# Kernel optimization log

Hardware: AMD Instinct MI355X
Metric: run time of the kernel (lower is better)

Reference implementation:

```python
import jax, jax.numpy as jnp
import numpy as np

B, S, D, NL = 512, 200, 128, 2
N_ITEMS = 50001
DH = 2 * D
DFF = 4 * D


def layer_norm(x, g, b, eps=1e-5):
    mu = x.mean(-1, keepdims=True)
    v = ((x - mu) ** 2).mean(-1, keepdims=True)
    return (x - mu) / jnp.sqrt(v + eps) * g + b


def lru_scan(h, lamb0, mask):
    # h: (B, L, DH) complex64, lamb0: (DH,) complex64, mask: (B, L) bool
    Bb, L, Dh = h.shape
    log2_L = int(np.ceil(np.log2(L)))
    lamb = lamb0.reshape(1, Dh)
    for i in range(1, log2_L + 1):
        l = 2 ** i
        h = h.reshape(Bb * L // l, l, Dh)
        m = mask.reshape(Bb * L // l, l)
        h1, h2 = h[:, : l // 2], h[:, l // 2:]
        if i > 1:
            lamb = jnp.concatenate([lamb, lamb * lamb[-1]], axis=0)  # powers lambda^1..lambda^(l/2)
        carry_gate = m[:, l // 2 - 1 : l // 2, None].astype(h.dtype)
        h2 = h2 + lamb * h1[:, -1:] * carry_gate
        h = jnp.concatenate([h1, h2], axis=1)
    return h.reshape(Bb, L, Dh)


def _forward(token_emb, emb_ln_g, emb_ln_b, params_log,
             in_wr, in_wi, in_br, in_bi, out_wr, out_wi, out_br, out_bi,
             lru_ln_g, lru_ln_b, w1, b1, w2, b2, ffn_ln_g, ffn_ln_b,
             item_seq, item_seq_len):
    mask = item_seq > 0                      # (B, S)
    x = token_emb[item_seq]                  # (B, S, D)
    x = layer_norm(x, emb_ln_g, emb_ln_b)
    seq_len = item_seq.shape[1]
    L = 2 ** int(np.ceil(np.log2(seq_len)))
    pad = L - seq_len
    x = jnp.pad(x, ((0, 0), (pad, 0), (0, 0)))        # left-pad seq to power of 2
    m = jnp.pad(mask, ((0, 0), (pad, 0)))
    n_layers = params_log.shape[0]
    for li in range(n_layers):
        pl = jnp.exp(params_log[li])                  # (3, DH): nu, theta, gamma
        nu, theta, gamma = pl[0], pl[1], pl[2]
        lamb0 = jnp.exp(jax.lax.complex(-nu, theta))  # (DH,)
        in_w = jax.lax.complex(in_wr[li], in_wi[li])
        in_b = jax.lax.complex(in_br[li], in_bi[li])
        h = (jnp.einsum('bld,hd->blh', x.astype(jnp.complex64), in_w) + in_b) * gamma
        h = lru_scan(h, lamb0, m)
        out_w = jax.lax.complex(out_wr[li], out_wi[li])
        out_b = jax.lax.complex(out_br[li], out_bi[li])
        y = (jnp.einsum('blh,dh->bld', h, out_w) + out_b).real + x
        x = layer_norm(y, lru_ln_g[li], lru_ln_b[li])
        # positionwise FFN with residual + post-LN
        hff = jax.nn.gelu(jnp.einsum('bld,fd->blf', x, w1[li]) + b1[li], approximate=False)
        x = layer_norm(jnp.einsum('blf,df->bld', hff, w2[li]) + b2[li] + x,
                       ffn_ln_g[li], ffn_ln_b[li])
    x = x[:, -seq_len:]                               # (B, S, D)
    idx = item_seq_len - 1
    return x[jnp.arange(x.shape[0]), idx]             # (B, D)


def setup_inputs() -> dict:
    key = jax.random.key(0)
    ks = jax.random.split(key, 24)
    std = 0.02
    item_seq = jax.random.randint(ks[0], (B, S), 0, N_ITEMS)
    item_seq_len = jax.random.randint(ks[1], (B,), 1, S + 1)
    # LRU diagonal init (matches torch init)
    r_min, r_max = 0.8, 0.99
    u1 = jax.random.uniform(ks[2], (NL, DH))
    u2 = jax.random.uniform(ks[3], (NL, DH))
    nu_log = jnp.log(-0.5 * jnp.log(u1 * (r_max ** 2 - r_min ** 2) + r_min ** 2))
    theta_log = jnp.log(u2 * 2.0 * np.pi)
    gamma_log = 0.5 * jnp.log(1.0 - jnp.exp(-2.0 * jnp.exp(nu_log)))
    params_log = jnp.stack([nu_log, theta_log, gamma_log], axis=1)  # (NL, 3, DH)
    rn = lambda k, sh: jax.random.normal(k, sh, dtype=jnp.float32) * std
    return {
        'token_emb': rn(ks[4], (N_ITEMS, D)),
        'emb_ln_g': jnp.ones((D,), jnp.float32), 'emb_ln_b': jnp.zeros((D,), jnp.float32),
        'params_log': params_log,
        'in_wr': rn(ks[5], (NL, DH, D)), 'in_wi': rn(ks[6], (NL, DH, D)),
        'in_br': rn(ks[7], (NL, DH)), 'in_bi': rn(ks[8], (NL, DH)),
        'out_wr': rn(ks[9], (NL, D, DH)), 'out_wi': rn(ks[10], (NL, D, DH)),
        'out_br': rn(ks[11], (NL, D)), 'out_bi': rn(ks[12], (NL, D)),
        'lru_ln_g': jnp.ones((NL, D), jnp.float32), 'lru_ln_b': jnp.zeros((NL, D), jnp.float32),
        'w1': rn(ks[13], (NL, DFF, D)), 'b1': rn(ks[14], (NL, DFF)),
        'w2': rn(ks[15], (NL, D, DFF)), 'b2': rn(ks[16], (NL, D)),
        'ffn_ln_g': jnp.ones((NL, D), jnp.float32), 'ffn_ln_b': jnp.zeros((NL, D), jnp.float32),
        'item_seq': item_seq, 'item_seq_len': item_seq_len,
    }


def reference(token_emb, emb_ln_g, emb_ln_b, params_log,
              in_wr, in_wi, in_br, in_bi, out_wr, out_wi, out_br, out_bi,
              lru_ln_g, lru_ln_b, w1, b1, w2, b2, ffn_ln_g, ffn_ln_b,
              item_seq, item_seq_len):
    return _forward(token_emb, emb_ln_g, emb_ln_b, params_log,
                    in_wr, in_wi, in_br, in_bi, out_wr, out_wi, out_br, out_bi,
                    lru_ln_g, lru_ln_b, w1, b1, w2, b2, ffn_ln_g, ffn_ln_b,
                    item_seq, item_seq_len)
```

## Files before the change

### kernel.cpp

```cpp
#include <hip/hip_runtime.h>
#include <hip/hip_bf16.h>
#include <math.h>

#define B_TOT 512
#define SEQ   200
#define D     128
#define DH    256
#define DFF   512
#define LPAD  256
#define PADL  56
#define NLAY  2
#define SSTRIP 140

typedef __attribute__((ext_vector_type(8))) short bf16x8;
typedef __attribute__((ext_vector_type(4))) float floatx4;
typedef __attribute__((ext_vector_type(2))) float floatx2;

static __device__ inline float bf2f(ushort u) {
    union { unsigned int i; float f; } v; v.i = ((unsigned int)u) << 16; return v.f;
}
static __device__ inline ushort f2bf(float x) {
    union { float f; unsigned int i; } v; v.f = x;
    unsigned int r = (v.i + 0x7FFFu + ((v.i >> 16) & 1u)) >> 16;
    return (ushort)r;
}
static __device__ inline unsigned int pkbf(float a, float b) {
    union { __hip_bfloat162 h; unsigned int u; } v;
    v.h = __float22bfloat162_rn(make_float2(a, b));
    return v.u;
}
static __device__ inline void gld_lds16(const void* g, void* l) {
    __builtin_amdgcn_global_load_lds(
        (const __attribute__((address_space(1))) unsigned int*)g,
        (__attribute__((address_space(3))) unsigned int*)l, 16, 0, 0);
}

static __device__ inline size_t haddr(int b, int s, int k) {
    int p  = k >> 8;
    int ch = k & 255;
    int g  = ch >> 5;
    int cl = ch & 31;
    return (((((size_t)b * 8 + g) * 2 + p) * SEQ + s) * 32 + cl);
}

__global__ void setup_all_kernel(const float* __restrict__ params_log,
                                 const float* __restrict__ in_br,
                                 const float* __restrict__ in_bi,
                                 const float* __restrict__ in_wr,
                                 const float* __restrict__ in_wi,
                                 const float* __restrict__ out_wr,
                                 const float* __restrict__ out_wi,
                                 const float* __restrict__ w1,
                                 const float* __restrict__ w2,
                                 ushort* __restrict__ Winb,
                                 ushort* __restrict__ W2effb,
                                 ushort* __restrict__ w1b,
                                 ushort* __restrict__ w2b,
                                 float* __restrict__ lam_pow,
                                 float* __restrict__ scale_in,
                                 float* __restrict__ bias_in)
{
    int idx = blockIdx.x * blockDim.x + threadIdx.x;
    int li = idx >> 16;
    int e  = idx & 65535;

    {
        int gp = e >> 12, rem = e & 4095;
        int q = rem >> 3, e8 = rem & 7;
        int r = q >> 4, cs = q & 15;
        int c16 = cs ^ (r & 7);
        int n = (r < 16) ? (gp * 16 + r) : (256 + gp * 16 + (r - 16));
        int d = c16 * 8 + e8;
        float wv = (n < DH) ? in_wr[((size_t)li * DH + n) * D + d]
                            : in_wi[((size_t)li * DH + (n - DH)) * D + d];
        Winb[idx] = f2bf(wv);
    }
    {
        int k0c = e >> 13, rem = e & 8191;
        int q = rem >> 3, e8 = rem & 7;
        int r = q >> 3, cs = q & 7;
        int c16 = cs ^ (r & 7);
        int k = k0c * 64 + c16 * 8 + e8;
        float w2v = (k < DH) ? out_wr[((size_t)li * D + r) * DH + k]
                             : -out_wi[((size_t)li * D + r) * DH + (k - DH)];
        W2effb[idx] = f2bf(w2v);
    }
    {
        int row = e >> 7, col = e & 127;
        int ffc = row >> 7, rl = row & 127;
        int c16 = col >> 3, e8 = col & 7;
        int cs = c16 ^ (rl & 7);
        w1b[li * 65536 + ffc * 16384 + rl * 128 + cs * 8 + e8] = f2bf(w1[idx]);
    }
    {
        int dd2 = e >> 9, kk = e & 511;
        int ffc = kk >> 7, klc = kk & 127;
        int c16 = klc >> 3, e8 = klc & 7;
        int cs = c16 ^ (dd2 & 7);
        w2b[li * 65536 + ffc * 16384 + dd2 * 128 + cs * 8 + e8] = f2bf(w2[idx]);
    }

    if (blockIdx.x < NLAY) {
        int pli = blockIdx.x;
        int c = threadIdx.x;
        const float* pl = params_log + (size_t)pli * 3 * DH;
        float nu = expf(pl[c]);
        float th = expf(pl[DH + c]);
        float ga = expf(pl[2 * DH + c]);
        float mag = expf(-nu);
        float lr = mag * cosf(th);
        float lim = mag * sinf(th);
        float2* lp = (float2*)(lam_pow + (size_t)pli * 65536) + (size_t)c * 128;
        float pr = lr, pi = lim;
        lp[0] = make_float2(pr, pi);
        for (int k = 1; k < 128; ++k) {
            float nr = pr * lr - pi * lim;
            float ni = pr * lim + pi * lr;
            pr = nr; pi = ni;
            lp[k] = make_float2(pr, pi);
        }
        scale_in[pli * 2 * DH + c]      = ga;
        scale_in[pli * 2 * DH + DH + c] = ga;
        bias_in[pli * 2 * DH + c]       = in_br[pli * DH + c] * ga;
        bias_in[pli * 2 * DH + DH + c]  = in_bi[pli * DH + c] * ga;
    }
}

__global__ __launch_bounds__(256) void embed_ln_kernel(
    const float* __restrict__ emb, const int* __restrict__ seq,
    const int* __restrict__ lenp,
    const float* __restrict__ g, const float* __restrict__ bt,
    ushort* __restrict__ x,
    int Bc, int* __restrict__ total, int* __restrict__ rowmap)
{
    if (blockIdx.x == gridDim.x - 1) {
        __shared__ int ps[257];
        int t = threadIdx.x;
        int b0_ = 2 * t, b1_ = 2 * t + 1;
        int lv0 = (b0_ < Bc) ? lenp[b0_] : 0;
        int lv1 = (b1_ < Bc) ? lenp[b1_] : 0;
        ps[t + 1] = lv0 + lv1;
        if (t == 0) ps[0] = 0;
        __syncthreads();
        for (int ofs = 1; ofs < 256; ofs <<= 1) {
            int v = ps[t + 1];
            int vv = (t + 1 > ofs) ? ps[t + 1 - ofs] : 0;
            __syncthreads();
            ps[t + 1] = v + vv;
            __syncthreads();
        }
        if (t == 255) total[0] = ps[256];
        int base = ps[t];
        int rb0 = b0_ * SEQ, rb1 = b1_ * SEQ;
        for (int s = 0; s < lv0; ++s) rowmap[base + s] = rb0 + s;
        base += lv0;
        for (int s = 0; s < lv1; ++s) rowmap[base + s] = rb1 + s;
        return;
    }
    int row  = blockIdx.x * 4 + (threadIdx.x >> 6);
    int lane = threadIdx.x & 63;
    int b = row / SEQ, s = row - b * SEQ;
    if (s >= lenp[b]) return;
    int item = seq[row];
    float2 v = *(const float2*)(emb + (size_t)item * D + lane * 2);
    float ssum = v.x + v.y;
#pragma unroll
    for (int o = 32; o > 0; o >>= 1) ssum += __shfl_xor(ssum, o);
    float mu = ssum * (1.0f / D);
    float d0 = v.x - mu, d1 = v.y - mu;
    float vs = d0 * d0 + d1 * d1;
#pragma unroll
    for (int o = 32; o > 0; o >>= 1) vs += __shfl_xor(vs, o);
    float rstd = rsqrtf(vs * (1.0f / D) + 1e-5f);
    float2 gg = *(const float2*)(g + lane * 2);
    float2 bb = *(const float2*)(bt + lane * 2);
    unsigned int o2 = pkbf(d0 * rstd * gg.x + bb.x, d1 * rstd * gg.y + bb.y);
    *(unsigned int*)(x + (size_t)row * D + lane * 2) = o2;
}

template <bool LAST>
__global__ __launch_bounds__(512) void inproj_scan_kernel(
    const ushort* __restrict__ X, const ushort* __restrict__ Win,
    ushort* __restrict__ H, const float2* __restrict__ lamT,
    const int* __restrict__ seq, const int* __restrict__ lenp,
    const float* __restrict__ scale_in, const float* __restrict__ bias_in)
{
    __shared__ __align__(16) char smem[36864];
    __shared__ __align__(16) float mkfS[32 * 12];
    char*  Wsm = smem;
    char*  xs  = smem + 8192;
    float* stR2 = (float*)smem;
    float* stI2 = stR2 + 32 * SSTRIP;

    int gp = blockIdx.x, b = blockIdx.y;
    int tid = threadIdx.x;
    int l = tid & 63, w = tid >> 6;
    int ct = w & 1;
    int rq = w >> 1;
    int lr = l & 15, lq = l >> 4;
    int wbase = tid & ~63;

    int c  = tid >> 5;
    int tl = tid & 31;
    int t0 = tl * 8;
    int lbase = l & 32;
    int coff = (c >> 2) * 36 + (c & 3) * 8;

    int s_b = lenp[b] - 1;
    int tile_max = s_b >> 4;
    int nrows = (tile_max + 1) * 16;
    int tb = s_b + PADL;
    bool activeT = (t0 <= tb);

    const ushort* xrow = X + (size_t)b * SEQ * 128;
    gld_lds16(Win + (size_t)gp * 4096 + (size_t)tid * 8,
              Wsm + (size_t)wbase * 16);
    int nrA = nrows < 112 ? nrows : 112;
#pragma unroll
    for (int it = 0; it < 4; ++it) {
        int rbase = it * 32 + w * 4;
        int r = rbase + lq;
        int cs = lr ^ (r & 7);
        if (r < nrA)
            gld_lds16(xrow + (size_t)r * 128 + cs * 8, xs + rbase * 256);
    }

    const float2* myl = lamT + (size_t)(gp * 16 + c) * 128;

    if (tid < LPAD) {
        int t = tid;
        float m = 0.f;
        if (t >= PADL) m = (seq[(size_t)b * SEQ + (t - PADL)] > 0) ? 1.f : 0.f;
        mkfS[(t >> 3) * 12 + (t & 7)] = m;
    }
    __syncthreads();

    bf16x8 wf[4];
#pragma unroll
    for (int kk = 0; kk < 4; ++kk) {
        int ca = kk * 4 + lq;
        int wr = ct * 16 + lr;
        wf[kk] = *(const bf16x8*)(Wsm + wr * 256 + ((ca ^ (wr & 7)) * 16));
    }
    int tstart = rq ? (3 * rq + 1) : 0;
    int tcnt   = rq ? 3 : 4;
    floatx4 acc[4];
#pragma unroll
    for (int tt = 0; tt < 4; ++tt) acc[tt] = (floatx4)0.f;

    if (rq < 2) {
#pragma unroll
        for (int tt = 0; tt < 4; ++tt) {
            if (tt < tcnt && (tstart + tt) <= tile_max) {
                int t  = tstart + tt;
                int ar = t * 16 + lr;
#pragma unroll
                for (int kk = 0; kk < 4; ++kk) {
                    int ca = kk * 4 + lq;
                    bf16x8 af = *(const bf16x8*)(xs + ar * 256 + ((ca ^ (ar & 7)) * 16));
                    acc[tt] = __builtin_amdgcn_mfma_f32_16x16x32_bf16(wf[kk], af, acc[tt], 0, 0, 0);
                }
            }
        }
    }
    __syncthreads();

    if (nrows > 112) {
        int nrB = nrows < 200 ? nrows : 200;
#pragma unroll
        for (int it = 0; it < 3; ++it) {
            int rbase = it * 32 + w * 4;
            int rl_ = rbase + lq;
            int gr = 112 + rl_;
            int cs = lr ^ (rl_ & 7);
            if (gr < nrB)
                gld_lds16(xrow + (size_t)gr * 128 + cs * 8, xs + rbase * 256);
        }
    }
    __syncthreads();

    if (rq >= 2) {
#pragma unroll
        for (int tt = 0; tt < 4; ++tt) {
            if (tt < tcnt && (tstart + tt) <= tile_max) {
                int t  = tstart + tt;
                int ar = (t - 7) * 16 + lr;
#pragma unroll
                for (int kk = 0; kk < 4; ++kk) {
                    int ca = kk * 4 + lq;
                    bf16x8 af = *(const bf16x8*)(xs + ar * 256 + ((ca ^ (ar & 7)) * 16));
                    acc[tt] = __builtin_amdgcn_mfma_f32_16x16x32_bf16(wf[kk], af, acc[tt], 0, 0, 0);
                }
            }
        }
    }
    __syncthreads();

    float2 l14[4];
#pragma unroll
    for (int k = 0; k < 4; ++k) l14[k] = myl[k];
    float2 myl9 = myl[8];
    float2 lam_e[3];
#pragma unroll
    for (int i = 0; i < 3; ++i) {
        int half = 32 << i;
        int off = t0 & ((half << 1) - 1);
        int e = off - half;
        lam_e[i] = myl[e < 0 ? 0 : e];
    }
    float2 l7;
    l7.x = l14[3].x * l14[2].x - l14[3].y * l14[2].y;
    l7.y = l14[3].x * l14[2].y + l14[3].y * l14[2].x;

    for (int idx = tid; idx < 7 * SSTRIP; idx += 512) { stR2[idx] = 0.f; stI2[idx] = 0.f; }
    {
        float4 g4 = *(const float4*)(scale_in + ct * 256 + gp * 16 + lq * 4);
        float4 b4 = *(const float4*)(bias_in  + ct * 256 + gp * 16 + lq * 4);
        float* base = ct ? stI2 : stR2;
#pragma unroll
        for (int tt = 0; tt < 4; ++tt) {
            if (tt < tcnt && (tstart + tt) <= tile_max) {
                int t = tstart + tt;
                int s = t * 16 + lr;
                if (s <= s_b) {
                    float* dst = base + (2 * t + 7 + (lr >> 3)) * SSTRIP
                               + lq * 36 + (lr & 7);
                    dst[0]  = acc[tt][0] * g4.x + b4.x;
                    dst[8]  = acc[tt][1] * g4.y + b4.y;
                    dst[16] = acc[tt][2] * g4.z + b4.z;
                    dst[24] = acc[tt][3] * g4.w + b4.w;
                }
            }
        }
    }
    __syncthreads();

    floatx2 Xr[4], Xi[4], Mf[4];
    {
        const float* pr = stR2 + tl * SSTRIP + coff;
        const float* pi = stI2 + tl * SSTRIP + coff;
        floatx4 r0 = *(const floatx4*)pr;
        floatx4 r1 = *(const floatx4*)(pr + 4);
        floatx4 i0 = *(const floatx4*)pi;
        floatx4 i1 = *(const floatx4*)(pi + 4);
        floatx4 m0 = *(const floatx4*)(mkfS + tl * 12);
        floatx4 m1 = *(const floatx4*)(mkfS + tl * 12 + 4);
        Xr[0] = floatx2{r0[0], r0[1]}; Xr[1] = floatx2{r0[2], r0[3]};
        Xr[2] = floatx2{r1[0], r1[1]}; Xr[3] = floatx2{r1[2], r1[3]};
        Xi[0] = floatx2{i0[0], i0[1]}; Xi[1] = floatx2{i0[2], i0[3]};
        Xi[2] = floatx2{i1[0], i1[1]}; Xi[3] = floatx2{i1[2], i1[3]};
        Mf[0] = floatx2{m0[0], m0[1]}; Mf[1] = floatx2{m0[2], m0[3]};
        Mf[2] = floatx2{m1[0], m1[1]}; Mf[3] = floatx2{m1[2], m1[3]};
    }

    float l0x = l14[0].x, l0y = l14[0].y;
    floatx2 L01R = floatx2{l14[0].x, l14[1].x};
    floatx2 L01I = floatx2{l14[0].y, l14[1].y};
    floatx2 L23R = floatx2{l14[2].x, l14[3].x};
    floatx2 L23I = floatx2{l14[2].y, l14[3].y};

    if (activeT) {
#pragma unroll
        for (int p = 0; p < 4; ++p) {
            float sr = Xr[p].x * Mf[p].x, si = Xi[p].x * Mf[p].x;
            Xr[p].y += l0x * sr; Xr[p].y -= l0y * si;
            Xi[p].y += l0x * si; Xi[p].y += l0y * sr;
        }
#pragma unroll
        for (int p = 0; p < 2; ++p) {
            int sp_ = p * 2;
            float sr = Xr[sp_].y * Mf[sp_].y, si = Xi[sp_].y * Mf[sp_].y;
            Xr[sp_ + 1] += sr * L01R; Xr[sp_ + 1] -= si * L01I;
            Xi[sp_ + 1] += si * L01R; Xi[sp_ + 1] += sr * L01I;
        }
        {
            float sr = Xr[1].y * Mf[1].y, si = Xi[1].y * Mf[1].y;
            Xr[2] += sr * L01R; Xr[2] -= si * L01I;
            Xi[2] += si * L01R; Xi[2] += sr * L01I;
            Xr[3] += sr * L23R; Xr[3] -= si * L23I;
            Xi[3] += si * L23R; Xi[3] += sr * L23I;
        }
    }

    float x7r, x7i;
    if (activeT) { x7r = Xr[3].y; x7i = Xi[3].y; }
    else         { x7r = 0.f;     x7i = 0.f; }
    float Ctr = 0.f, Cti = 0.f;
    float m7 = Mf[3].y;
    float pxr = x7r * m7, pxi = x7i * m7;

#define TREE_LEVEL(SRC_TL, TGT, LE)                                          \
    {                                                                        \
        int srcl = lbase | (SRC_TL);                                         \
        float svx = __shfl(pxr, srcl);                                       \
        float svy = __shfl(pxi, srcl);                                       \
        if (activeT && (TGT)) {                                              \
            float2 le = (LE);                                                \
            float cr = le.x * svx - le.y * svy;                              \
            float ci = le.x * svy + le.y * svx;                              \
            Ctr += cr; Cti += ci;                                            \
            x7r += l7.x * cr - l7.y * ci;                                    \
            x7i += l7.x * ci + l7.y * cr;                                    \
            pxr = x7r * m7; pxi = x7i * m7;                                  \
        }                                                                    \
    }

    TREE_LEVEL(tl & ~1,          tl & 1,  l14[0]);
    TREE_LEVEL((tl & ~3)  | 1,   tl & 2,  (tl & 1) ? myl9 : l14[0]);
    TREE_LEVEL((tl & ~7)  | 3,   tl & 4,  lam_e[0]);
    if (tb >= 64)  TREE_LEVEL((tl & ~15) | 7,  tl & 8,  lam_e[1]);
    if (tb >= 128) TREE_LEVEL((tl & ~31) | 15, tl & 16, lam_e[2]);
#undef TREE_LEVEL

    if (activeT && (!LAST || (unsigned)(tb - t0) < 7u)) {
        float2 l5, l6;
        l5.x = l14[3].x * l14[0].x - l14[3].y * l14[0].y;
        l5.y = l14[3].x * l14[0].y + l14[3].y * l14[0].x;
        l6.x = l14[3].x * l14[1].x - l14[3].y * l14[1].y;
        l6.y = l14[3].x * l14[1].y + l14[3].y * l14[1].x;
        Xr[0].x += Ctr;                                 Xi[0].x += Cti;
        Xr[0].y += l14[0].x * Ctr; Xr[0].y -= l14[0].y * Cti;
        Xi[0].y += l14[0].x * Cti; Xi[0].y += l14[0].y * Ctr;
        Xr[1].x += l14[1].x * Ctr; Xr[1].x -= l14[1].y * Cti;
        Xi[1].x += l14[1].x * Cti; Xi[1].x += l14[1].y * Ctr;
        Xr[1].y += l14[2].x * Ctr; Xr[1].y -= l14[2].y * Cti;
        Xi[1].y += l14[2].x * Cti; Xi[1].y += l14[2].y * Ctr;
        Xr[2].x += l14[3].x * Ctr; Xr[2].x -= l14[3].y * Cti;
        Xi[2].x += l14[3].x * Cti; Xi[2].x += l14[3].y * Ctr;
        Xr[2].y += l5.x * Ctr;     Xr[2].y -= l5.y * Cti;
        Xi[2].y += l5.x * Cti;     Xi[2].y += l5.y * Ctr;
        Xr[3].x += l6.x * Ctr;     Xr[3].x -= l6.y * Cti;
        Xi[3].x += l6.x * Cti;     Xi[3].x += l6.y * Ctr;
    }
    Xr[3].y = x7r; Xi[3].y = x7i;

    if (LAST) {
        if (activeT && (unsigned)(tb - t0) < 8u) {
#pragma unroll
            for (int k = 0; k < 8; ++k)
                if (t0 + k == tb) {
                    float vr = (k & 1) ? Xr[k >> 1].y : Xr[k >> 1].x;
                    float vi = (k & 1) ? Xi[k >> 1].y : Xi[k >> 1].x;
                    stR2[tl * SSTRIP + coff + k] = vr;
                    stI2[tl * SSTRIP + coff + k] = vi;
                }
        }
    } else {
        if (activeT && tl >= 7) {
            floatx4 r0 = floatx4{Xr[0].x, Xr[0].y, Xr[1].x, Xr[1].y};
            floatx4 r1 = floatx4{Xr[2].x, Xr[2].y, Xr[3].x, Xr[3].y};
            floatx4 i0 = floatx4{Xi[0].x, Xi[0].y, Xi[1].x, Xi[1].y};
            floatx4 i1 = floatx4{Xi[2].x, Xi[2].y, Xi[3].x, Xi[3].y};
            *(floatx4*)(stR2 + tl * SSTRIP + coff)     = r0;
            *(floatx4*)(stR2 + tl * SSTRIP + coff + 4) = r1;
            *(floatx4*)(stI2 + tl * SSTRIP + coff)     = i0;
            *(floatx4*)(stI2 + tl * SSTRIP + coff + 4) = i1;
        }
    }
    __syncthreads();

    if (LAST) {
        if (tid < 32) {
            int p = tid >> 4, cc = tid & 15;
            int fi = (tb >> 3) * SSTRIP + (cc >> 2) * 36 + (cc & 3) * 8 + (tb & 7);
            float v = (p ? stI2 : stR2)[fi];
            H[(size_t)b * 512 + p * 256 + gp * 16 + cc] = f2bf(v);
        }
    } else {
        int g  = gp >> 1;
        int hc = (gp & 1) * 16;
        ushort* baseg = H + (size_t)(b * 8 + g) * 2 * SEQ * 32 + hc;
#pragma unroll
        for (int it = 0; it < 4; ++it) {
            int idx4 = it * 512 + tid;
            if (idx4 < 2 * SEQ * 4) {
                int q  = idx4 & 3;
                int ps = idx4 >> 2;
                int p  = ps >= SEQ;
                int s  = ps - p * SEQ;
                if (s > s_b) continue;
                const float* sp = (p ? stI2 : stR2)
                                + ((s + PADL) >> 3) * SSTRIP + q * 36 + (s & 7);
                float a0 = sp[0], a1 = sp[8], a2 = sp[16], a3 = sp[24];
                uint2 raw;
                raw.x = pkbf(a0, a1);
                raw.y = pkbf(a2, a3);
                *(uint2*)(baseg + (size_t)ps * 32 + q * 4) = raw;
            }
        }
    }
}

__global__ __launch_bounds__(256) void outproj_kernel(
    const ushort* __restrict__ A, const ushort* __restrict__ Wimg,
    ushort* __restrict__ Cout,
    const int* __restrict__ rowmap, const int* __restrict__ totalp,
    const float* __restrict__ e0,
    const ushort* __restrict__ res,
    const float* __restrict__ lng, const float* __restrict__ lnb)
{
    int m0 = blockIdx.x * 64;
    int total = totalp[0];
    if (m0 >= total) return;
    __shared__ __align__(16) char As[8192];
    __shared__ __align__(16) char Bs[16384];
    __shared__ float2 lnS[2][64];
    int tid = threadIdx.x;
    int l = tid & 63, w = tid >> 6;
    int chh = w >> 1;
    int rh  = w & 1;
    int lr = l & 15, lq = l >> 4;
    int wbase = tid & ~63;

    int cst = tid & 7;
    int rr  = tid >> 3;
    int sb[2], ss[2];
#pragma unroll
    for (int it = 0; it < 2; ++it) {
        int gr = m0 + it * 32 + rr;
        if (gr >= total) gr = total - 1;
        int rm = rowmap[gr];
        sb[it] = rm / SEQ; ss[it] = rm - sb[it] * SEQ;
    }

    floatx4 acc[4][2];
#pragma unroll
    for (int i = 0; i < 4; ++i)
#pragma unroll
        for (int j = 0; j < 2; ++j) acc[i][j] = (floatx4)0.f;

    for (int k0c = 0; k0c < 8; ++k0c) {
        int k0 = k0c * 64;
        {
            const ushort* img = Wimg + (size_t)k0c * 8192;
#pragma unroll
            for (int it = 0; it < 4; ++it)
                gld_lds16(img + (size_t)(it * 256 + tid) * 8,
                          Bs + (size_t)(it * 256 + wbase) * 16);
        }
#pragma unroll
        for (int it = 0; it < 2; ++it) {
            int r = it * 32 + rr;
            uint4 va = *(const uint4*)(A + haddr(sb[it], ss[it], k0 + cst * 8));
            *(uint4*)(As + r * 128 + ((cst ^ (r & 7)) * 16)) = va;
        }
        __syncthreads();
#pragma unroll
        for (int kk = 0; kk < 2; ++kk) {
            bf16x8 wf[4], af[2];
            int ca = kk * 4 + lq;
#pragma unroll
            for (int i = 0; i < 4; ++i) {
                int rb = chh * 64 + i * 16 + lr;
                wf[i] = *(const bf16x8*)(Bs + rb * 128 + ((ca ^ (rb & 7)) * 16));
            }
#pragma unroll
            for (int j = 0; j < 2; ++j) {
                int ra = rh * 32 + j * 16 + lr;
                af[j] = *(const bf16x8*)(As + ra * 128 + ((ca ^ (ra & 7)) * 16));
            }
#pragma unroll
            for (int i = 0; i < 4; ++i)
#pragma unroll
                for (int j = 0; j < 2; ++j)
                    acc[i][j] = __builtin_amdgcn_mfma_f32_16x16x32_bf16(
                        wf[i], af[j], acc[i][j], 0, 0, 0);
        }
        __syncthreads();
    }

    int chb[4], arow[2], rmj[2];
#pragma unroll
    for (int i = 0; i < 4; ++i) chb[i] = chh * 64 + i * 16 + lq * 4;
#pragma unroll
    for (int j = 0; j < 2; ++j) {
        arow[j] = m0 + rh * 32 + j * 16 + lr;
        int rc = arow[j] < total ? arow[j] : total - 1;
        rmj[j] = rowmap[rc];
    }

    {
        float4 bias[4], gv[4], bv[4];
#pragma unroll
        for (int i = 0; i < 4; ++i) {
            bias[i] = *(const float4*)(e0 + chb[i]);
            gv[i]   = *(const float4*)(lng + chb[i]);
            bv[i]   = *(const float4*)(lnb + chb[i]);
        }
#pragma unroll
        for (int j = 0; j < 2; ++j) {
#pragma unroll
            for (int i = 0; i < 4; ++i) {
                ushort4 r4 = *(const ushort4*)(res + (size_t)rmj[j] * 128 + chb[i]);
                acc[i][j][0] += ((const float*)&bias[i])[0] + bf2f(r4.x);
                acc[i][j][1] += ((const float*)&bias[i])[1] + bf2f(r4.y);
                acc[i][j][2] += ((const float*)&bias[i])[2] + bf2f(r4.z);
                acc[i][j][3] += ((const float*)&bias[i])[3] + bf2f(r4.w);
            }
        }
#pragma unroll
        for (int j = 0; j < 2; ++j) {
            float s = 0.f, q = 0.f;
#pragma unroll
            for (int i = 0; i < 4; ++i)
#pragma unroll
                for (int reg = 0; reg < 4; ++reg) {
                    float v = acc[i][j][reg];
                    s += v; q += v * v;
                }
            s += __shfl_xor(s, 16); q += __shfl_xor(q, 16);
            s += __shfl_xor(s, 32); q += __shfl_xor(q, 32);
            if (lq == 0) lnS[chh][rh * 32 + j * 16 + lr] = make_float2(s, q);
        }
        __syncthreads();
#pragma unroll
        for (int j = 0; j < 2; ++j) {
            int rl = rh * 32 + j * 16 + lr;
            float2 s0 = lnS[0][rl], s1 = lnS[1][rl];
            float mu  = (s0.x + s1.x) * (1.0f / 128.0f);
            float var = (s0.y + s1.y) * (1.0f / 128.0f) - mu * mu;
            float rstd = rsqrtf(var + 1e-5f);
            if (arow[j] < total) {
#pragma unroll
                for (int i = 0; i < 4; ++i) {
                    uint2 u;
                    u.x = pkbf((acc[i][j][0] - mu) * rstd * ((const float*)&gv[i])[0] + ((const float*)&bv[i])[0],
                               (acc[i][j][1] - mu) * rstd * ((const float*)&gv[i])[1] + ((const float*)&bv[i])[1]);
                    u.y = pkbf((acc[i][j][2] - mu) * rstd * ((const float*)&gv[i])[2] + ((const float*)&bv[i])[2],
                               (acc[i][j][3] - mu) * rstd * ((const float*)&gv[i])[3] + ((const float*)&bv[i])[3]);
                    *(uint2*)(Cout + (size_t)rmj[j] * 128 + chb[i]) = u;
                }
            }
        }
    }
}

__global__ __launch_bounds__(256) void outproj_last_kernel(
    const ushort* __restrict__ Hc, const ushort* __restrict__ Wimg,
    ushort* __restrict__ xc, int Bc,
    const float* __restrict__ e0,
    const ushort* __restrict__ Xres, const int* __restrict__ lenp,
    const float* __restrict__ lng, const float* __restrict__ lnb)
{
    __shared__ __align__(16) char As[8192];
    __shared__ __align__(16) char Bs[16384];
    __shared__ float2 lnS[2][64];
    int tid = threadIdx.x;
    int l = tid & 63, w = tid >> 6;
    int chh = w >> 1;
    int rh  = w & 1;
    int lr = l & 15, lq = l >> 4;
    int m0 = blockIdx.x * 64;
    int wbase = tid & ~63;

    int cst = tid & 7;
    int rr  = tid >> 3;

    floatx4 acc[4][2];
#pragma unroll
    for (int i = 0; i < 4; ++i)
#pragma unroll
        for (int j = 0; j < 2; ++j) acc[i][j] = (floatx4)0.f;

    for (int k0c = 0; k0c < 8; ++k0c) {
        int k0 = k0c * 64;
        {
            const ushort* img = Wimg + (size_t)k0c * 8192;
#pragma unroll
            for (int it = 0; it < 4; ++it)
                gld_lds16(img + (size_t)(it * 256 + tid) * 8,
                          Bs + (size_t)(it * 256 + wbase) * 16);
        }
#pragma unroll
        for (int it = 0; it < 2; ++it) {
            int r = it * 32 + rr;
            int gr = m0 + r; if (gr >= Bc) gr = Bc - 1;
            uint4 va = *(const uint4*)(Hc + (size_t)gr * 512 + k0 + cst * 8);
            *(uint4*)(As + r * 128 + ((cst ^ (r & 7)) * 16)) = va;
        }
        __syncthreads();
#pragma unroll
        for (int kk = 0; kk < 2; ++kk) {
            bf16x8 wf[4], af[2];
            int ca = kk * 4 + lq;
#pragma unroll
            for (int i = 0; i < 4; ++i) {
                int rb = chh * 64 + i * 16 + lr;
                wf[i] = *(const bf16x8*)(Bs + rb * 128 + ((ca ^ (rb & 7)) * 16));
            }
#pragma unroll
            for (int j = 0; j < 2; ++j) {
                int ra = rh * 32 + j * 16 + lr;
                af[j] = *(const bf16x8*)(As + ra * 128 + ((ca ^ (ra & 7)) * 16));
            }
#pragma unroll
            for (int i = 0; i < 4; ++i)
#pragma unroll
                for (int j = 0; j < 2; ++j)
                    acc[i][j] = __builtin_amdgcn_mfma_f32_16x16x32_bf16(
                        wf[i], af[j], acc[i][j], 0, 0, 0);
        }
        __syncthreads();
    }

    int chb[4], arow[2];
#pragma unroll
    for (int i = 0; i < 4; ++i) chb[i] = chh * 64 + i * 16 + lq * 4;
#pragma unroll
    for (int j = 0; j < 2; ++j) arow[j] = m0 + rh * 32 + j * 16 + lr;

    {
        float4 bias[4], gv[4], bv[4];
#pragma unroll
        for (int i = 0; i < 4; ++i) {
            bias[i] = *(const float4*)(e0 + chb[i]);
            gv[i]   = *(const float4*)(lng + chb[i]);
            bv[i]   = *(const float4*)(lnb + chb[i]);
        }
#pragma unroll
        for (int j = 0; j < 2; ++j) {
            int br = arow[j] < Bc ? arow[j] : Bc - 1;
            int sb_ = lenp[br] - 1;
            const ushort* rbase = Xres + ((size_t)br * SEQ + sb_) * 128;
#pragma unroll
            for (int i = 0; i < 4; ++i) {
                ushort4 r4 = *(const ushort4*)(rbase + chb[i]);
                acc[i][j][0] += ((const float*)&bias[i])[0] + bf2f(r4.x);
                acc[i][j][1] += ((const float*)&bias[i])[1] + bf2f(r4.y);
                acc[i][j][2] += ((const float*)&bias[i])[2] + bf2f(r4.z);
                acc[i][j][3] += ((const float*)&bias[i])[3] + bf2f(r4.w);
            }
        }
#pragma unroll
        for (int j = 0; j < 2; ++j) {
            float s = 0.f, q = 0.f;
#pragma unroll
            for (int i = 0; i < 4; ++i)
#pragma unroll
                for (int reg = 0; reg < 4; ++reg) {
                    float v = acc[i][j][reg];
                    s += v; q += v * v;
                }
            s += __shfl_xor(s, 16); q += __shfl_xor(q, 16);
            s += __shfl_xor(s, 32); q += __shfl_xor(q, 32);
            if (lq == 0) lnS[chh][rh * 32 + j * 16 + lr] = make_float2(s, q);
        }
        __syncthreads();
#pragma unroll
        for (int j = 0; j < 2; ++j) {
            int rl = rh * 32 + j * 16 + lr;
            float2 s0 = lnS[0][rl], s1 = lnS[1][rl];
            float mu  = (s0.x + s1.x) * (1.0f / 128.0f);
            float var = (s0.y + s1.y) * (1.0f / 128.0f) - mu * mu;
            float rstd = rsqrtf(var + 1e-5f);
            if (arow[j] < Bc) {
#pragma unroll
                for (int i = 0; i < 4; ++i) {
                    uint2 u;
                    u.x = pkbf((acc[i][j][0] - mu) * rstd * ((const float*)&gv[i])[0] + ((const float*)&bv[i])[0],
                               (acc[i][j][1] - mu) * rstd * ((const float*)&gv[i])[1] + ((const float*)&bv[i])[1]);
                    u.y = pkbf((acc[i][j][2] - mu) * rstd * ((const float*)&gv[i])[2] + ((const float*)&bv[i])[2],
                               (acc[i][j][3] - mu) * rstd * ((const float*)&gv[i])[3] + ((const float*)&bv[i])[3]);
                    *(uint2*)(xc + (size_t)arow[j] * 128 + chb[i]) = u;
                }
            }
        }
    }
}

__global__ __launch_bounds__(256) void ffn_fused_kernel(
    ushort* __restrict__ X, const ushort* __restrict__ W1,
    const ushort* __restrict__ W2,
    const float* __restrict__ b1, const float* __restrict__ b2,
    const float* __restrict__ lng, const float* __restrict__ lnb,
    int Mtot, const int* __restrict__ rowmap, const int* __restrict__ totalp,
    float* __restrict__ outp, int b0f)
{
    int m0 = blockIdx.x * 32;
    int total = totalp ? totalp[0] : Mtot;
    if (m0 >= total) return;
    __shared__ __align__(16) char Bs[2][32768];
    __shared__ ushort Ps[32 * 136];
    __shared__ float2 lnS[4][32];
    int tid = threadIdx.x;
    int l = tid & 63, w = tid >> 6;
    int chh = w;
    int lr = l & 15, lq = l >> 4;
    int wbase = tid & ~63;

    {
        const ushort* img = W1;
#pragma unroll
        for (int it = 0; it < 8; ++it)
            gld_lds16(img + (size_t)(it * 256 + tid) * 8,
                      Bs[0] + (size_t)(it * 256 + wbase) * 16);
    }

    int arow[2], rmrow[2];
#pragma unroll
    for (int j = 0; j < 2; ++j) {
        arow[j] = m0 + j * 16 + lr;
        int rc = arow[j] < total ? arow[j] : total - 1;
        rmrow[j] = rowmap ? rowmap[rc] : rc;
    }

    bf16x8 af_x[8];
#pragma unroll
    for (int j = 0; j < 2; ++j)
#pragma unroll
        for (int kk2 = 0; kk2 < 4; ++kk2) {
            int k = kk2 * 32 + lq * 8;
            af_x[(j << 2) | kk2] = *(const bf16x8*)(X + (size_t)rmrow[j] * 128 + k);
        }

    floatx4 acc2[2][2];
#pragma unroll
    for (int i = 0; i < 2; ++i)
#pragma unroll
        for (int j = 0; j < 2; ++j) acc2[i][j] = (floatx4)0.f;
    floatx4 acc1[2][2];

#pragma unroll
    for (int s = 0; s < 8; ++s) {
        __syncthreads();
        if (s < 7) {
            int sn = s + 1;
            const ushort* img = ((sn & 1) ? W2 : W1) + (size_t)(sn >> 1) * 16384;
            char* dst = Bs[sn & 1];
#pragma unroll
            for (int it = 0; it < 8; ++it)
                gld_lds16(img + (size_t)(it * 256 + tid) * 8,
                          dst + (size_t)(it * 256 + wbase) * 16);
        }
        const char* B = Bs[s & 1];
        int ffc = s >> 1;
        if (!(s & 1)) {
#pragma unroll
            for (int i = 0; i < 2; ++i)
#pragma unroll
                for (int j = 0; j < 2; ++j) acc1[i][j] = (floatx4)0.f;
#pragma unroll
            for (int kk2 = 0; kk2 < 4; ++kk2) {
                int ca = kk2 * 4 + lq;
                bf16x8 wf[2];
#pragma unroll
                for (int i = 0; i < 2; ++i) {
                    int rb = chh * 32 + i * 16 + lr;
                    wf[i] = *(const bf16x8*)(B + rb * 256 + ((ca ^ (rb & 7)) * 16));
                }
#pragma unroll
                for (int i = 0; i < 2; ++i)
#pragma unroll
                    for (int j = 0; j < 2; ++j)
                        acc1[i][j] = __builtin_amdgcn_mfma_f32_16x16x32_bf16(
                            wf[i], af_x[(j << 2) | kk2], acc1[i][j], 0, 0, 0);
            }
#pragma unroll
            for (int j = 0; j < 2; ++j) {
                int rowl = j * 16 + lr;
#pragma unroll
                for (int i = 0; i < 2; ++i) {
                    int ch0 = chh * 32 + i * 16 + lq * 4;
                    float4 bv = *(const float4*)(b1 + ffc * 128 + ch0);
                    float g0, g1, g2, g3, v;
                    v = acc1[i][j][0] + bv.x; g0 = 0.5f * v * (1.0f + erff(v * 0.70710678118654752f));
                    v = acc1[i][j][1] + bv.y; g1 = 0.5f * v * (1.0f + erff(v * 0.70710678118654752f));
                    v = acc1[i][j][2] + bv.z; g2 = 0.5f * v * (1.0f + erff(v * 0.70710678118654752f));
                    v = acc1[i][j][3] + bv.w; g3 = 0.5f * v * (1.0f + erff(v * 0.70710678118654752f));
                    uint2 u; u.x = pkbf(g0, g1); u.y = pkbf(g2, g3);
                    *(uint2*)(Ps + rowl * 136 + ch0) = u;
                }
            }
        } else {
#pragma unroll
            for (int kk2 = 0; kk2 < 4; ++kk2) {
                int ca = kk2 * 4 + lq;
                bf16x8 wf[2], af[2];
#pragma unroll
                for (int i = 0; i < 2; ++i) {
                    int rb = chh * 32 + i * 16 + lr;
                    wf[i] = *(const bf16x8*)(B + rb * 256 + ((ca ^ (rb & 7)) * 16));
                }
#pragma unroll
                for (int j = 0; j < 2; ++j) {
                    int rowl = j * 16 + lr;
                    af[j] = *(const bf16x8*)(Ps + rowl * 136 + kk2 * 32 + lq * 8);
                }
#pragma unroll
                for (int i = 0; i < 2; ++i)
#pragma unroll
                    for (int j = 0; j < 2; ++j)
                        acc2[i][j] = __builtin_amdgcn_mfma_f32_16x16x32_bf16(
                            wf[i], af[j], acc2[i][j], 0, 0, 0);
            }
        }
    }

    int chb[2];
#pragma unroll
    for (int i = 0; i < 2; ++i) chb[i] = chh * 32 + i * 16 + lq * 4;

    float4 bias[2], gv[2], bv[2];
#pragma unroll
    for (int i = 0; i < 2; ++i) {
        bias[i] = *(const float4*)(b2 + chb[i]);
        gv[i]   = *(const float4*)(lng + chb[i]);
        bv[i]   = *(const float4*)(lnb + chb[i]);
    }
#pragma unroll
    for (int j = 0; j < 2; ++j) {
#pragma unroll
        for (int i = 0; i < 2; ++i) {
            ushort4 r4 = *(const ushort4*)(X + (size_t)rmrow[j] * 128 + chb[i]);
            acc2[i][j][0] += ((const float*)&bias[i])[0] + bf2f(r4.x);
            acc2[i][j][1] += ((const float*)&bias[i])[1] + bf2f(r4.y);
            acc2[i][j][2] += ((const float*)&bias[i])[2] + bf2f(r4.z);
            acc2[i][j][3] += ((const float*)&bias[i])[3] + bf2f(r4.w);
        }
    }
#pragma unroll
    for (int j = 0; j < 2; ++j) {
        float s = 0.f, q = 0.f;
#pragma unroll
        for (int i = 0; i < 2; ++i)
#pragma unroll
            for (int reg = 0; reg < 4; ++reg) {
                float v = acc2[i][j][reg];
                s += v; q += v * v;
            }
        s += __shfl_xor(s, 16); q += __shfl_xor(q, 16);
        s += __shfl_xor(s, 32); q += __shfl_xor(q, 32);
        if (lq == 0) lnS[chh][j * 16 + lr] = make_float2(s, q);
    }
    __syncthreads();
#pragma unroll
    for (int j = 0; j < 2; ++j) {
        int rl = j * 16 + lr;
        float2 s0 = lnS[0][rl], s1 = lnS[1][rl];
        float2 s2 = lnS[2][rl], s3 = lnS[3][rl];
        float mu  = (s0.x + s1.x + s2.x + s3.x) * (1.0f / 128.0f);
        float var = (s0.y + s1.y + s2.y + s3.y) * (1.0f / 128.0f) - mu * mu;
        float rstd = rsqrtf(var + 1e-5f);
        if (arow[j] < total) {
            if (outp) {
#pragma unroll
                for (int i = 0; i < 2; ++i) {
                    float4 o;
                    o.x = (acc2[i][j][0] - mu) * rstd * ((const float*)&gv[i])[0] + ((const float*)&bv[i])[0];
                    o.y = (acc2[i][j][1] - mu) * rstd * ((const float*)&gv[i])[1] + ((const float*)&bv[i])[1];
                    o.z = (acc2[i][j][2] - mu) * rstd * ((const float*)&gv[i])[2] + ((const float*)&bv[i])[2];
                    o.w = (acc2[i][j][3] - mu) * rstd * ((const float*)&gv[i])[3] + ((const float*)&bv[i])[3];
                    *(float4*)(outp + (size_t)(b0f + rmrow[j]) * 128 + chb[i]) = o;
                }
            } else {
#pragma unroll
                for (int i = 0; i < 2; ++i) {
                    uint2 u;
                    u.x = pkbf((acc2[i][j][0] - mu) * rstd * ((const float*)&gv[i])[0] + ((const float*)&bv[i])[0],
                               (acc2[i][j][1] - mu) * rstd * ((const float*)&gv[i])[1] + ((const float*)&bv[i])[1]);
                    u.y = pkbf((acc2[i][j][2] - mu) * rstd * ((const float*)&gv[i])[2] + ((const float*)&bv[i])[2],
                               (acc2[i][j][3] - mu) * rstd * ((const float*)&gv[i])[3] + ((const float*)&bv[i])[3]);
                    *(uint2*)(X + (size_t)rmrow[j] * 128 + chb[i]) = u;
                }
            }
        }
    }
}

extern "C" void kernel_launch(void* const* d_in, const int* in_sizes, int n_in,
                              void* d_out, int out_size, void* d_ws, size_t ws_size,
                              hipStream_t stream)
{
    const float* token_emb  = (const float*)d_in[0];
    const float* emb_ln_g   = (const float*)d_in[1];
    const float* emb_ln_b   = (const float*)d_in[2];
    const float* params_log = (const float*)d_in[3];
    const float* in_wr      = (const float*)d_in[4];
    const float* in_wi      = (const float*)d_in[5];
    const float* in_br      = (const float*)d_in[6];
    const float* in_bi      = (const float*)d_in[7];
    const float* out_wr     = (const float*)d_in[8];
    const float* out_wi     = (const float*)d_in[9];
    const float* out_br     = (const float*)d_in[10];
    const float* lru_ln_g   = (const float*)d_in[12];
    const float* lru_ln_b   = (const float*)d_in[13];
    const float* w1         = (const float*)d_in[14];
    const float* b1         = (const float*)d_in[15];
    const float* w2         = (const float*)d_in[16];
    const float* b2         = (const float*)d_in[17];
    const float* ffn_ln_g   = (const float*)d_in[18];
    const float* ffn_ln_b   = (const float*)d_in[19];
    const int*   item_seq   = (const int*)d_in[20];
    const int*   item_seq_len = (const int*)d_in[21];
    float* out = (float*)d_out;

    char* ws = (char*)d_ws;
    ushort* Winb   = (ushort*)ws;                      ws += NLAY * 65536 * 2;
    ushort* W2effb = (ushort*)ws;                      ws += NLAY * 65536 * 2;
    ushort* w1b    = (ushort*)ws;                      ws += NLAY * 65536 * 2;
    ushort* w2b    = (ushort*)ws;                      ws += NLAY * 65536 * 2;
    float* lam_pow = (float*)ws;                       ws += NLAY * 65536 * 4;
    float* scale_in = (float*)ws;                      ws += NLAY * 512 * 4;
    float* bias_in  = (float*)ws;                      ws += NLAY * 512 * 4;
    size_t table_bytes = (size_t)(ws - (char*)d_ws);

    int Bc = B_TOT;
    while (Bc > 32) {
        size_t need = table_bytes
                    + (size_t)Bc * SEQ * (D * 2 + 2 * DH * 2)
                    + (size_t)(Bc * SEQ + 8) * 4 + 1024;
        if (need <= ws_size) break;
        Bc >>= 1;
    }
    ushort* xb = (ushort*)ws;                          ws += (size_t)Bc * SEQ * D * 2;
    ushort* hb = (ushort*)ws;                          ws += (size_t)Bc * SEQ * 2 * DH * 2;
    int* totalp = (int*)ws;                            ws += 8 * 4;
    int* rowmap = (int*)ws;
    ushort* Hc = hb;
    ushort* xc = hb + (size_t)Bc * 512;

    setup_all_kernel<<<NLAY * 65536 / 256, 256, 0, stream>>>(
        params_log, in_br, in_bi, in_wr, in_wi, out_wr, out_wi, w1, w2,
        Winb, W2effb, w1b, w2b, lam_pow, scale_in, bias_in);

    for (int b0 = 0; b0 < B_TOT; b0 += Bc) {
        int M = Bc * SEQ;
        const int* lenp = item_seq_len + b0;
        embed_ln_kernel<<<M / 4 + 1, 256, 0, stream>>>(
            token_emb, item_seq + (size_t)b0 * SEQ, lenp,
            emb_ln_g, emb_ln_b, xb, Bc, totalp, rowmap);

        for (int li = 0; li < NLAY; ++li) {
            if (li < NLAY - 1) {
                inproj_scan_kernel<false><<<dim3(16, Bc), 512, 0, stream>>>(
                    xb, Winb + (size_t)li * 65536, hb,
                    (const float2*)(lam_pow + (size_t)li * 65536),
                    item_seq + (size_t)b0 * SEQ, lenp,
                    scale_in + li * 512, bias_in + li * 512);
                outproj_kernel<<<dim3(M / 64), 256, 0, stream>>>(
                    hb, W2effb + (size_t)li * 65536, xb, rowmap, totalp,
                    out_br + li * D, xb,
                    lru_ln_g + li * D, lru_ln_b + li * D);
                ffn_fused_kernel<<<dim3(M / 32), 256, 0, stream>>>(
                    xb, w1b + (size_t)li * 65536, w2b + (size_t)li * 65536,
                    b1 + li * DFF, b2 + li * D,
                    ffn_ln_g + li * D, ffn_ln_b + li * D, M, rowmap, totalp,
                    (float*)0, 0);
            } else {
                inproj_scan_kernel<true><<<dim3(16, Bc), 512, 0, stream>>>(
                    xb, Winb + (size_t)li * 65536, Hc,
                    (const float2*)(lam_pow + (size_t)li * 65536),
                    item_seq + (size_t)b0 * SEQ, lenp,
                    scale_in + li * 512, bias_in + li * 512);
                outproj_last_kernel<<<dim3((Bc + 63) / 64), 256, 0, stream>>>(
                    Hc, W2effb + (size_t)li * 65536, xc, Bc,
                    out_br + li * D, xb, lenp,
                    lru_ln_g + li * D, lru_ln_b + li * D);
                ffn_fused_kernel<<<dim3((Bc + 31) / 32), 256, 0, stream>>>(
                    xc, w1b + (size_t)li * 65536, w2b + (size_t)li * 65536,
                    b1 + li * DFF, b2 + li * D,
                    ffn_ln_g + li * D, ffn_ln_b + li * D, Bc,
                    (const int*)0, (const int*)0, out, b0);
            }
        }
    }
}
```

Baseline: 374.6 us.

## Double-buffer out-projection LDS tiles and swizzle scan block order

Both out-projection GEMM kernels now use two LDS buffers, so the next K chunk's weights (via direct global-to-LDS loads) and activations (via registers) are fetched while MFMAs run on the current chunk. This removes one barrier per iteration and hides global load latency, at the cost of doubled LDS per block, which may reduce occupancy. Separately, the in-projection/scan kernel remaps its flattened block index with an 8-way swizzle that changes which (group, batch) pairs run together, likely aiming at better cache or XCD locality.

```diff
diff --git a/kernel.cpp b/kernel.cpp
--- a/kernel.cpp
+++ b/kernel.cpp
@@ -192,7 +192,11 @@
     float* stR2 = (float*)smem;
     float* stI2 = stR2 + 32 * SSTRIP;
 
-    int gp = blockIdx.x, b = blockIdx.y;
+    int flat = blockIdx.y * 16 + blockIdx.x;
+    int cpx  = (gridDim.y * 16) >> 3;
+    int swz  = (flat & 7) * cpx + (flat >> 3);
+    int gp = swz & 15, b = swz >> 4;
+
     int tid = threadIdx.x;
     int l = tid & 63, w = tid >> 6;
     int ct = w & 1;
@@ -502,8 +506,8 @@
     int m0 = blockIdx.x * 64;
     int total = totalp[0];
     if (m0 >= total) return;
-    __shared__ __align__(16) char As[8192];
-    __shared__ __align__(16) char Bs[16384];
+    __shared__ __align__(16) char As[2][8192];
+    __shared__ __align__(16) char Bs[2][16384];
     __shared__ float2 lnS[2][64];
     int tid = threadIdx.x;
     int l = tid & 63, w = tid >> 6;
@@ -523,6 +527,20 @@
         sb[it] = rm / SEQ; ss[it] = rm - sb[it] * SEQ;
     }
 
+    {
+#pragma unroll
+        for (int it = 0; it < 4; ++it)
+            gld_lds16(Wimg + (size_t)(it * 256 + tid) * 8,
+                      Bs[0] + (size_t)(it * 256 + wbase) * 16);
+#pragma unroll
+        for (int it = 0; it < 2; ++it) {
+            int r = it * 32 + rr;
+            uint4 va = *(const uint4*)(A + haddr(sb[it], ss[it], cst * 8));
+            *(uint4*)(As[0] + r * 128 + ((cst ^ (r & 7)) * 16)) = va;
+        }
+    }
+    __syncthreads();
+
     floatx4 acc[4][2];
 #pragma unroll
     for (int i = 0; i < 4; ++i)
@@ -530,21 +548,21 @@
         for (int j = 0; j < 2; ++j) acc[i][j] = (floatx4)0.f;
 
     for (int k0c = 0; k0c < 8; ++k0c) {
-        int k0 = k0c * 64;
-        {
-            const ushort* img = Wimg + (size_t)k0c * 8192;
+        int cur = k0c & 1, nb = cur ^ 1;
+        uint4 van[2];
+        if (k0c < 7) {
+            const ushort* img = Wimg + (size_t)(k0c + 1) * 8192;
 #pragma unroll
             for (int it = 0; it < 4; ++it)
                 gld_lds16(img + (size_t)(it * 256 + tid) * 8,
-                          Bs + (size_t)(it * 256 + wbase) * 16);
-        }
-#pragma unroll
-        for (int it = 0; it < 2; ++it) {
-            int r = it * 32 + rr;
-            uint4 va = *(const uint4*)(A + haddr(sb[it], ss[it], k0 + cst * 8));
-            *(uint4*)(As + r * 128 + ((cst ^ (r & 7)) * 16)) = va;
-        }
-        __syncthreads();
+                          Bs[nb] + (size_t)(it * 256 + wbase) * 16);
+#pragma unroll
+            for (int it = 0; it < 2; ++it)
+                van[it] = *(const uint4*)(A + haddr(sb[it], ss[it],
+                                                   (k0c + 1) * 64 + cst * 8));
+        }
+        const char* Asb = As[cur];
+        const char* Bsb = Bs[cur];
 #pragma unroll
         for (int kk = 0; kk < 2; ++kk) {
             bf16x8 wf[4], af[2];
@@ -552,12 +570,12 @@
 #pragma unroll
             for (int i = 0; i < 4; ++i) {
                 int rb = chh * 64 + i * 16 + lr;
-                wf[i] = *(const bf16x8*)(Bs + rb * 128 + ((ca ^ (rb & 7)) * 16));
+                wf[i] = *(const bf16x8*)(Bsb + rb * 128 + ((ca ^ (rb & 7)) * 16));
             }
 #pragma unroll
             for (int j = 0; j < 2; ++j) {
                 int ra = rh * 32 + j * 16 + lr;
-                af[j] = *(const bf16x8*)(As + ra * 128 + ((ca ^ (ra & 7)) * 16));
+                af[j] = *(const bf16x8*)(Asb + ra * 128 + ((ca ^ (ra & 7)) * 16));
             }
 #pragma unroll
             for (int i = 0; i < 4; ++i)
@@ -565,6 +583,13 @@
                 for (int j = 0; j < 2; ++j)
                     acc[i][j] = __builtin_amdgcn_mfma_f32_16x16x32_bf16(
                         wf[i], af[j], acc[i][j], 0, 0, 0);
+        }
+        if (k0c < 7) {
+#pragma unroll
+            for (int it = 0; it < 2; ++it) {
+                int r = it * 32 + rr;
+                *(uint4*)(As[nb] + r * 128 + ((cst ^ (r & 7)) * 16)) = van[it];
+            }
         }
         __syncthreads();
     }
@@ -642,8 +667,8 @@
     const ushort* __restrict__ Xres, const int* __restrict__ lenp,
     const float* __restrict__ lng, const float* __restrict__ lnb)
 {
-    __shared__ __align__(16) char As[8192];
-    __shared__ __align__(16) char Bs[16384];
+    __shared__ __align__(16) char As[2][8192];
+    __shared__ __align__(16) char Bs[2][16384];
     __shared__ float2 lnS[2][64];
     int tid = threadIdx.x;
     int l = tid & 63, w = tid >> 6;
@@ -655,6 +680,26 @@
 
     int cst = tid & 7;
     int rr  = tid >> 3;
+    int gr2[2];
+#pragma unroll
+    for (int it = 0; it < 2; ++it) {
+        int gr = m0 + it * 32 + rr;
+        gr2[it] = gr < Bc ? gr : Bc - 1;
+    }
+
+    {
+#pragma unroll
+        for (int it = 0; it < 4; ++it)
+            gld_lds16(Wimg + (size_t)(it * 256 + tid) * 8,
+                      Bs[0] + (size_t)(it * 256 + wbase) * 16);
+#pragma unroll
+        for (int it = 0; it < 2; ++it) {
+            int r = it * 32 + rr;
+            uint4 va = *(const uint4*)(Hc + (size_t)gr2[it] * 512 + cst * 8);
+            *(uint4*)(As[0] + r * 128 + ((cst ^ (r & 7)) * 16)) = va;
+        }
+    }
+    __syncthreads();
 
     floatx4 acc[4][2];
 #pragma unroll
@@ -663,22 +708,21 @@
         for (int j = 0; j < 2; ++j) acc[i][j] = (floatx4)0.f;
 
     for (int k0c = 0; k0c < 8; ++k0c) {
-        int k0 = k0c * 64;
-        {
-            const ushort* img = Wimg + (size_t)k0c * 8192;
+        int cur = k0c & 1, nb = cur ^ 1;
+        uint4 van[2];
+        if (k0c < 7) {
+            const ushort* img = Wimg + (size_t)(k0c + 1) * 8192;
 #pragma unroll
             for (int it = 0; it < 4; ++it)
                 gld_lds16(img + (size_t)(it * 256 + tid) * 8,
-                          Bs + (size_t)(it * 256 + wbase) * 16);
-        }
-#pragma unroll
-        for (int it = 0; it < 2; ++it) {
-            int r = it * 32 + rr;
-            int gr = m0 + r; if (gr >= Bc) gr = Bc - 1;
-            uint4 va = *(const uint4*)(Hc + (size_t)gr * 512 + k0 + cst * 8);
-            *(uint4*)(As + r * 128 + ((cst ^ (r & 7)) * 16)) = va;
-        }
-        __syncthreads();
+                          Bs[nb] + (size_t)(it * 256 + wbase) * 16);
+#pragma unroll
+            for (int it = 0; it < 2; ++it)
+                van[it] = *(const uint4*)(Hc + (size_t)gr2[it] * 512
+                                          + (k0c + 1) * 64 + cst * 8);
+        }
+        const char* Asb = As[cur];
+        const char* Bsb = Bs[cur];
 #pragma unroll
         for (int kk = 0; kk < 2; ++kk) {
             bf16x8 wf[4], af[2];
@@ -686,12 +730,12 @@
 #pragma unroll
             for (int i = 0; i < 4; ++i) {
                 int rb = chh * 64 + i * 16 + lr;
-                wf[i] = *(const bf16x8*)(Bs + rb * 128 + ((ca ^ (rb & 7)) * 16));
+                wf[i] = *(const bf16x8*)(Bsb + rb * 128 + ((ca ^ (rb & 7)) * 16));
             }
 #pragma unroll
             for (int j = 0; j < 2; ++j) {
                 int ra = rh * 32 + j * 16 + lr;
-                af[j] = *(const bf16x8*)(As + ra * 128 + ((ca ^ (ra & 7)) * 16));
+                af[j] = *(const bf16x8*)(Asb + ra * 128 + ((ca ^ (ra & 7)) * 16));
             }
 #pragma unroll
             for (int i = 0; i < 4; ++i)
@@ -699,6 +743,13 @@
                 for (int j = 0; j < 2; ++j)
                     acc[i][j] = __builtin_amdgcn_mfma_f32_16x16x32_bf16(
                         wf[i], af[j], acc[i][j], 0, 0, 0);
+        }
+        if (k0c < 7) {
+#pragma unroll
+            for (int it = 0; it < 2; ++it) {
+                int r = it * 32 + rr;
+                *(uint4*)(As[nb] + r * 128 + ((cst ^ (r & 7)) * 16)) = van[it];
+            }
         }
         __syncthreads();
     }
```

Result: no change. 374.7 us (+0.0%).
